# Kernel optimization log

Measured on AMD Instinct MI355X. Metric: run time of the kernel, lower is better.

Reference implementation:

```python
import jax, jax.numpy as jnp
import numpy as np

MAX_SX = 10  # max_shiftx
MAX_SY = 10  # max_shifty
STD_EPS = 1e-9


def setup_inputs() -> dict:
    key = jax.random.key(0)
    x = jax.random.normal(key, (8, 32, 128, 128), dtype=jnp.float32)
    return {"x": x}


def _cross_correlation(x):
    b, c, h, w = x.shape
    n = h * w
    # _standartize: zero-mean, divide by (unbiased std * sqrt(h*w)); std<eps -> inf -> 0
    xc = x - jnp.mean(x, axis=(2, 3), keepdims=True)
    std = jnp.std(xc, axis=(2, 3), keepdims=True, ddof=1)
    std = jnp.where(std < STD_EPS, jnp.inf, std)
    xs = xc / (std * jnp.sqrt(jnp.asarray(n, x.dtype)))
    # FFT-based circular cross-correlation for all ordered pairs (i, j>=i)
    Xf = jnp.fft.fft2(xs)  # [b, c, h, w] complex
    ii, jj = np.triu_indices(c)  # row-major: (0,0),(0,1),...,(0,c-1),(1,1),... matches the loop order
    cross = Xf[:, ii] * jnp.conj(Xf[:, jj])  # [b, P, h, w], P = c*(c+1)//2
    cc = jnp.real(jnp.fft.ifft2(cross))
    # The [[br, bl], [tr, tl]] corner concat == roll by (sy, sx) then take leading window
    cc = jnp.roll(cc, (MAX_SY, MAX_SX), axis=(2, 3))
    return cc[:, :, : 2 * MAX_SY + 1, : 2 * MAX_SX + 1]  # [b, P, 2sy+1, 2sx+1]


def reference(x):
    return _cross_correlation(x)
```

## Files before the change

kernel.cpp:

```cpp
#include <hip/hip_runtime.h>
#include <hip/hip_bf16.h>

typedef __attribute__((ext_vector_type(4))) unsigned int uint4v;
typedef __attribute__((ext_vector_type(8))) short short8;
typedef __attribute__((ext_vector_type(16))) float floatx16;

#define NROWP 152
#define ROWB2 12288
#define BB2   ((size_t)NROWP*ROWB2)
#define COPYB ((size_t)8*BB2)
#define STATS_OFF ((size_t)2*COPYB)
#define ABUF (38*2048)
#define LDS_BYTES (2*ABUF)

__device__ __forceinline__ unsigned short f2b(float f){
  unsigned int u = __float_as_uint(f);
  return (unsigned short)((u + 0x7fffu + ((u >> 16) & 1u)) >> 16);
}

__device__ __forceinline__ void gload_lds16(const void* g, void* l){
  __builtin_amdgcn_global_load_lds((const __attribute__((address_space(1))) unsigned int*)g,
                                   (__attribute__((address_space(3))) unsigned int*)l, 16, 0, 0);
}

__global__ __launch_bounds__(256) void k_stat(const float* __restrict__ x,
                                              float* __restrict__ stats){
  int bid = blockIdx.x;
  int t = threadIdx.x;
  const float* xc = x + ((size_t)bid << 14);
  float s = 0.f, ss = 0.f;
  #pragma unroll 4
  for (int k = 0; k < 64; ++k){
    float v = xc[t + (k << 8)];
    s += v; ss += v*v;
  }
  #pragma unroll
  for (int m = 32; m >= 1; m >>= 1){
    s  += __shfl_xor(s, m);
    ss += __shfl_xor(ss, m);
  }
  __shared__ float rs[4], rss[4];
  int wv = t >> 6, l = t & 63;
  if (l == 0){ rs[wv] = s; rss[wv] = ss; }
  __syncthreads();
  if (t == 0){
    float S  = rs[0]+rs[1]+rs[2]+rs[3];
    float SS = rss[0]+rss[1]+rss[2]+rss[3];
    float mean = S * (1.f/16384.f);
    float var  = (SS - S*mean) * (1.f/16383.f);
    float sd = sqrtf(fmaxf(var, 0.f));
    stats[bid*2]   = mean;
    stats[bid*2+1] = (sd < 1e-9f) ? 0.f : 1.f/(sd*128.f);
  }
}

__global__ __launch_bounds__(512) void k_pack(const float* __restrict__ x,
                                              const float* __restrict__ stats,
                                              unsigned char* __restrict__ pad){
  __shared__ float rowbuf[32*129];
  int bid = blockIdx.x;
  int b = bid & 7, rg = bid >> 3;
  int t = threadIdx.x;
  int ch = t >> 4, xq = t & 15;
  float mean  = stats[(b*32 + ch)*2];
  float scale = stats[(b*32 + ch)*2 + 1];
  const float* xc = x + ((size_t)(b*32 + ch) << 14);
  for (int rr = 0; rr < 4; ++rr){
    int r = rg*4 + rr;
    int sy = (r + 118) & 127;
    const float* src = xc + (sy << 7) + (xq << 3);
    float4 v0 = *(const float4*)src;
    float4 v1 = *(const float4*)(src + 4);
    float* rb = rowbuf + ch*129 + (xq << 3);
    rb[0] = (v0.x-mean)*scale; rb[1] = (v0.y-mean)*scale;
    rb[2] = (v0.z-mean)*scale; rb[3] = (v0.w-mean)*scale;
    rb[4] = (v1.x-mean)*scale; rb[5] = (v1.y-mean)*scale;
    rb[6] = (v1.z-mean)*scale; rb[7] = (v1.w-mean)*scale;
    __syncthreads();
    #pragma unroll
    for (int k = 0; k < 3; ++k){
      int u = t + (k << 9);
      int pp = (u >= 768) ? 1 : 0;
      int u2 = u - 768*pp;
      int xi = u2 / 192;
      int u3 = u2 - 192*xi;
      int cq = u3 / 6;
      int seg = u3 - 6*cq;
      const float* rbq = rowbuf + cq*129;
      int x0 = 32*xi + 8*seg + pp;
      unsigned int d[4];
      #pragma unroll
      for (int e = 0; e < 4; ++e){
        unsigned int lo = f2b(rbq[(x0 + 2*e)     & 127]);
        unsigned int hi = f2b(rbq[(x0 + 2*e + 1) & 127]);
        d[e] = lo | (hi << 16);
      }
      uint4v ov = {d[0], d[1], d[2], d[3]};
      *(uint4v*)(pad + (size_t)pp*COPYB + ((size_t)(b*NROWP + r))*ROWB2
                 + (unsigned)(xi*3072 + cq*96 + seg*16)) = ov;
    }
    __syncthreads();
  }
}

__global__ __launch_bounds__(512, 1) void k_corr(const unsigned char* __restrict__ pad,
                                                 float* __restrict__ out){
  extern __shared__ char lds[];
  float* sf = (float*)lds;

  int bid = blockIdx.x;
  int b = bid & 7, cg = bid >> 3;
  int dx, d0;
  if (cg < 2){ dx = 0; d0 = cg << 2; }
  else { int q = cg - 2; dx = 1 + q/3; d0 = -10 + 7*(q - 3*(q/3)); }
  int p = dx & 1, dxe = dx - p;

  int tid = threadIdx.x;
  int lane = tid & 63, wvi = tid >> 6;
  int ks = wvi & 1, kq = wvi >> 1;
  unsigned offF = (unsigned)(ks*1024 + ((lane >> 5) << 9) + ((lane & 31) << 4));
  unsigned oA = (unsigned)((lane & 31)*96 + 2*dxe);
  unsigned oB = (unsigned)((lane & 31)*96 + 16*(2*ks + (lane >> 5)));

  const unsigned char* baseA = pad + (size_t)p*COPYB + (size_t)b*BB2;
  const unsigned char* baseB = pad + (size_t)b*BB2;

  floatx16 acc[7];
  #pragma unroll
  for (int d = 0; d < 7; ++d) acc[d] = (floatx16)(0.0f);

  auto stageA = [&](int tt, char* buf){
    int rab = 32*(tt >> 2) + 10 + d0;
    unsigned xio = (unsigned)((tt & 3)*3072);
    #pragma unroll
    for (int s = 0; s < 10; ++s){
      int u = wvi + (s << 3);
      if (s < 9 || wvi < 4){
        int row = u >> 1, cp = u & 1;
        const unsigned char* g = baseA + (size_t)(rab + row)*ROWB2 + xio
                                 + oA + (unsigned)(16*(2*cp + (lane >> 5)));
        gload_lds16(g, buf + (unsigned)(row*2048 + cp*1024 + lane*16));
      }
    }
  };
  auto pBrow = [&](int tt)->const unsigned char*{
    return baseB + (size_t)(32*(tt >> 2) + 10 + kq*8)*ROWB2
                 + (unsigned)((tt & 3)*3072) + oB;
  };

  stageA(0, lds);
  __builtin_amdgcn_sched_barrier(0);
  short8 BQ[4];
  {
    const unsigned char* pB0 = pBrow(0);
    #pragma unroll
    for (int k = 0; k < 4; ++k) __builtin_memcpy(&BQ[k], pB0 + (size_t)k*ROWB2, 16);
  }
  __builtin_amdgcn_sched_barrier(0);
  asm volatile("s_waitcnt vmcnt(4)" ::: "memory");
  __builtin_amdgcn_sched_barrier(0);
  __builtin_amdgcn_s_barrier();
  __builtin_amdgcn_sched_barrier(0);

  for (int t = 0; t < 16; ++t){
    if (t < 15) stageA(t+1, lds + ((t+1)&1)*ABUF);
    __builtin_amdgcn_sched_barrier(0);
    const char* Ab = lds + (t&1)*ABUF + (kq*8)*2048 + offF;
    const unsigned char* pBc = pBrow(t);
    const unsigned char* pBn = pBrow(t+1);
    bool more = (t < 15);
    short8 ring[8];
    #pragma unroll
    for (int w = 0; w < 8; ++w) ring[w] = *(const short8*)(Ab + w*2048);
    __builtin_amdgcn_s_setprio(1);
    #pragma unroll
    for (int yl = 0; yl < 8; ++yl){
      short8 bf = BQ[yl & 3];
      #pragma unroll
      for (int d = 0; d < 7; ++d)
        acc[d] = __builtin_amdgcn_mfma_f32_32x32x16_bf16(ring[(yl+d)&7], bf, acc[d], 0, 0, 0);
      if (yl < 4)       __builtin_memcpy(&BQ[yl & 3], pBc + (size_t)(yl + 4)*ROWB2, 16);
      else if (more)    __builtin_memcpy(&BQ[yl & 3], pBn + (size_t)(yl - 4)*ROWB2, 16);
      if (yl < 6) ring[yl & 7] = *(const short8*)(Ab + (yl + 8)*2048);
    }
    __builtin_amdgcn_s_setprio(0);
    __builtin_amdgcn_sched_barrier(0);
    asm volatile("s_waitcnt vmcnt(4) lgkmcnt(0)" ::: "memory");
    __builtin_amdgcn_sched_barrier(0);
    __builtin_amdgcn_s_barrier();
    __builtin_amdgcn_sched_barrier(0);
  }

  int baseb = b * 232848;
  #pragma unroll
  for (int d = 0; d < 7; ++d){
    #pragma unroll
    for (int r = 0; r < 16; ++r)
      sf[wvi*1024 + r*64 + lane] = acc[d][r];
    __syncthreads();
    int dy = d0 + d;
    #pragma unroll
    for (int k = 0; k < 2; ++k){
      int pp0 = tid + (k << 9);
      float v = 0.f;
      #pragma unroll
      for (int w = 0; w < 8; ++w) v += sf[w*1024 + pp0];
      int reg = pp0 >> 6, ln = pp0 & 63;
      int i = (reg & 3) + 8*(reg >> 2) + 4*(ln >> 5);
      int j = ln & 31;
      if (i <= j){
        int pp = i*(65 - i)/2 + (j - i);
        out[baseb + pp*441 + (10+dy)*21 + (10+dx)] = v;
        if (i == j && (dy != 0 || dx != 0))
          out[baseb + pp*441 + (10-dy)*21 + (10-dx)] = v;
      } else {
        int pp = j*(65 - j)/2 + (i - j);
        out[baseb + pp*441 + (10-dy)*21 + (10-dx)] = v;
      }
    }
    __syncthreads();
  }
}

extern "C" void kernel_launch(void* const* d_in, const int* in_sizes, int n_in,
                              void* d_out, int out_size, void* d_ws, size_t ws_size,
                              hipStream_t stream){
  const float* x = (const float*)d_in[0];
  unsigned char* pad = (unsigned char*)d_ws;
  float* stats = (float*)((char*)d_ws + STATS_OFF);
  float* out = (float*)d_out;
  hipFuncSetAttribute((const void*)k_corr, hipFuncAttributeMaxDynamicSharedMemorySize,
                      LDS_BYTES);
  k_stat<<<dim3(256), dim3(256), 0, stream>>>(x, stats);
  k_pack<<<dim3(304), dim3(512), 0, stream>>>(x, stats, pad);
  k_corr<<<dim3(256), dim3(512), LDS_BYTES, stream>>>(pad, out);
}
```

Before: 82.56 us.

## Interleave A-tile staging with MFMA phases using barrier-synchronized ping-pong schedule

Splits each iteration's A-tile global-to-LDS staging into four chunks, each issued between pairs of MFMA steps, with workgroup barriers separating the memory and compute phases. This is a ping-pong style schedule meant to overlap global loads with matrix math and spread memory traffic evenly. It adds several barriers per iteration, which can cost synchronization time. It also changes the vmcnt wait accounting, which could hurt correctness or throughput if the counts are off.

Result: no change. 83.16 us (+0.7%).

```diff
diff --git a/kernel.cpp b/kernel.cpp
--- a/kernel.cpp
+++ b/kernel.cpp
@@ -12,6 +12,8 @@
 #define STATS_OFF ((size_t)2*COPYB)
 #define ABUF (38*2048)
 #define LDS_BYTES (2*ABUF)
+
+#define SB __builtin_amdgcn_sched_barrier(0)
 
 __device__ __forceinline__ unsigned short f2b(float f){
   unsigned int u = __float_as_uint(f);
@@ -129,18 +131,14 @@
   #pragma unroll
   for (int d = 0; d < 7; ++d) acc[d] = (floatx16)(0.0f);
 
-  auto stageA = [&](int tt, char* buf){
-    int rab = 32*(tt >> 2) + 10 + d0;
-    unsigned xio = (unsigned)((tt & 3)*3072);
-    #pragma unroll
-    for (int s = 0; s < 10; ++s){
-      int u = wvi + (s << 3);
-      if (s < 9 || wvi < 4){
-        int row = u >> 1, cp = u & 1;
-        const unsigned char* g = baseA + (size_t)(rab + row)*ROWB2 + xio
-                                 + oA + (unsigned)(16*(2*cp + (lane >> 5)));
-        gload_lds16(g, buf + (unsigned)(row*2048 + cp*1024 + lane*16));
-      }
+  auto stageUnit = [&](int tt, char* buf, int s){
+    int u = wvi + (s << 3);
+    if (u < 76){
+      int row = u >> 1, cp = u & 1;
+      int rab = 32*(tt >> 2) + 10 + d0;
+      const unsigned char* g = baseA + (size_t)(rab + row)*ROWB2
+            + (unsigned)((tt & 3)*3072) + oA + (unsigned)(16*(2*cp + (lane >> 5)));
+      gload_lds16(g, buf + (unsigned)(row*2048 + cp*1024 + lane*16));
     }
   };
   auto pBrow = [&](int tt)->const unsigned char*{
@@ -148,47 +146,74 @@
                  + (unsigned)((tt & 3)*3072) + oB;
   };
 
-  stageA(0, lds);
-  __builtin_amdgcn_sched_barrier(0);
+  #pragma unroll
+  for (int s = 0; s < 10; ++s) stageUnit(0, lds, s);
+  SB;
   short8 BQ[4];
   {
     const unsigned char* pB0 = pBrow(0);
     #pragma unroll
     for (int k = 0; k < 4; ++k) __builtin_memcpy(&BQ[k], pB0 + (size_t)k*ROWB2, 16);
   }
-  __builtin_amdgcn_sched_barrier(0);
+  SB;
   asm volatile("s_waitcnt vmcnt(4)" ::: "memory");
-  __builtin_amdgcn_sched_barrier(0);
-  __builtin_amdgcn_s_barrier();
-  __builtin_amdgcn_sched_barrier(0);
+  SB; __builtin_amdgcn_s_barrier(); SB;
 
   for (int t = 0; t < 16; ++t){
-    if (t < 15) stageA(t+1, lds + ((t+1)&1)*ABUF);
-    __builtin_amdgcn_sched_barrier(0);
     const char* Ab = lds + (t&1)*ABUF + (kq*8)*2048 + offF;
+    char* nbuf = lds + ((t+1)&1)*ABUF;
     const unsigned char* pBc = pBrow(t);
     const unsigned char* pBn = pBrow(t+1);
     bool more = (t < 15);
     short8 ring[8];
-    #pragma unroll
-    for (int w = 0; w < 8; ++w) ring[w] = *(const short8*)(Ab + w*2048);
-    __builtin_amdgcn_s_setprio(1);
-    #pragma unroll
-    for (int yl = 0; yl < 8; ++yl){
+    auto STEP = [&](int yl){
       short8 bf = BQ[yl & 3];
       #pragma unroll
       for (int d = 0; d < 7; ++d)
         acc[d] = __builtin_amdgcn_mfma_f32_32x32x16_bf16(ring[(yl+d)&7], bf, acc[d], 0, 0, 0);
-      if (yl < 4)       __builtin_memcpy(&BQ[yl & 3], pBc + (size_t)(yl + 4)*ROWB2, 16);
-      else if (more)    __builtin_memcpy(&BQ[yl & 3], pBn + (size_t)(yl - 4)*ROWB2, 16);
-      if (yl < 6) ring[yl & 7] = *(const short8*)(Ab + (yl + 8)*2048);
-    }
-    __builtin_amdgcn_s_setprio(0);
-    __builtin_amdgcn_sched_barrier(0);
-    asm volatile("s_waitcnt vmcnt(4) lgkmcnt(0)" ::: "memory");
-    __builtin_amdgcn_sched_barrier(0);
-    __builtin_amdgcn_s_barrier();
-    __builtin_amdgcn_sched_barrier(0);
+    };
+    #pragma unroll
+    for (int w = 0; w < 8; ++w) ring[w] = *(const short8*)(Ab + w*2048);
+    if (more){ stageUnit(t+1,nbuf,0); stageUnit(t+1,nbuf,1); stageUnit(t+1,nbuf,2); }
+    SB; __builtin_amdgcn_s_barrier();
+    asm volatile("s_waitcnt lgkmcnt(0)" ::: "memory"); SB;
+    __builtin_amdgcn_s_setprio(1); STEP(0); STEP(1); __builtin_amdgcn_s_setprio(0);
+    __builtin_memcpy(&BQ[0], pBc + (size_t)4*ROWB2, 16);
+    __builtin_memcpy(&BQ[1], pBc + (size_t)5*ROWB2, 16);
+    SB; __builtin_amdgcn_s_barrier(); SB;
+    ring[0] = *(const short8*)(Ab + 8*2048);
+    ring[1] = *(const short8*)(Ab + 9*2048);
+    if (more){ stageUnit(t+1,nbuf,3); stageUnit(t+1,nbuf,4); stageUnit(t+1,nbuf,5); }
+    SB; __builtin_amdgcn_s_barrier();
+    asm volatile("s_waitcnt lgkmcnt(0)" ::: "memory"); SB;
+    __builtin_amdgcn_s_setprio(1); STEP(2); STEP(3); __builtin_amdgcn_s_setprio(0);
+    __builtin_memcpy(&BQ[2], pBc + (size_t)6*ROWB2, 16);
+    __builtin_memcpy(&BQ[3], pBc + (size_t)7*ROWB2, 16);
+    SB; __builtin_amdgcn_s_barrier(); SB;
+    ring[2] = *(const short8*)(Ab + 10*2048);
+    ring[3] = *(const short8*)(Ab + 11*2048);
+    if (more){ stageUnit(t+1,nbuf,6); stageUnit(t+1,nbuf,7); }
+    SB; __builtin_amdgcn_s_barrier();
+    asm volatile("s_waitcnt lgkmcnt(0)" ::: "memory"); SB;
+    __builtin_amdgcn_s_setprio(1); STEP(4); STEP(5); __builtin_amdgcn_s_setprio(0);
+    if (more){
+      __builtin_memcpy(&BQ[0], pBn, 16);
+      __builtin_memcpy(&BQ[1], pBn + (size_t)ROWB2, 16);
+    }
+    SB; __builtin_amdgcn_s_barrier(); SB;
+    ring[4] = *(const short8*)(Ab + 12*2048);
+    ring[5] = *(const short8*)(Ab + 13*2048);
+    if (more){ stageUnit(t+1,nbuf,8); stageUnit(t+1,nbuf,9); }
+    SB; __builtin_amdgcn_s_barrier();
+    asm volatile("s_waitcnt lgkmcnt(0)" ::: "memory"); SB;
+    __builtin_amdgcn_s_setprio(1); STEP(6); STEP(7); __builtin_amdgcn_s_setprio(0);
+    if (more){
+      __builtin_memcpy(&BQ[2], pBn + (size_t)2*ROWB2, 16);
+      __builtin_memcpy(&BQ[3], pBn + (size_t)3*ROWB2, 16);
+    }
+    SB;
+    if (more){ asm volatile("s_waitcnt vmcnt(2)" ::: "memory"); }
+    SB; __builtin_amdgcn_s_barrier(); SB;
   }
 
   int baseb = b * 232848;
```

## Fuse channel statistics into pack and apply normalization algebraically in epilogue

Applied to the files above, without the earlier changes.

Removes the separate statistics kernel that re-read the whole input: the pack kernel now stores raw bf16 values and accumulates per-channel partial sums and sums of squares. A tiny single-block kernel reduces those partials to mean and scale. The correlation epilogue then corrects each output as (sum - N*mean_i*mean_j)*scale_i*scale_j. This saves a full pass over the input, at the cost of an extra small serial launch and some precision risk, since raw values rather than centered ones are rounded to bf16.

Result: faster. 79.19 us (-4.1%).

```diff
diff --git a/kernel.cpp b/kernel.cpp
--- a/kernel.cpp
+++ b/kernel.cpp
@@ -9,9 +9,12 @@
 #define ROWB2 12288
 #define BB2   ((size_t)NROWP*ROWB2)
 #define COPYB ((size_t)8*BB2)
-#define STATS_OFF ((size_t)2*COPYB)
+#define PART_OFF ((size_t)2*COPYB)
+#define STATS_OFF (PART_OFF + 304*32*2*4)
 #define ABUF (38*2048)
 #define LDS_BYTES (2*ABUF)
+
+#define SB __builtin_amdgcn_sched_barrier(0)
 
 __device__ __forceinline__ unsigned short f2b(float f){
   unsigned int u = __float_as_uint(f);
@@ -23,59 +26,30 @@
                                    (__attribute__((address_space(3))) unsigned int*)l, 16, 0, 0);
 }
 
-__global__ __launch_bounds__(256) void k_stat(const float* __restrict__ x,
-                                              float* __restrict__ stats){
-  int bid = blockIdx.x;
-  int t = threadIdx.x;
-  const float* xc = x + ((size_t)bid << 14);
-  float s = 0.f, ss = 0.f;
-  #pragma unroll 4
-  for (int k = 0; k < 64; ++k){
-    float v = xc[t + (k << 8)];
-    s += v; ss += v*v;
-  }
-  #pragma unroll
-  for (int m = 32; m >= 1; m >>= 1){
-    s  += __shfl_xor(s, m);
-    ss += __shfl_xor(ss, m);
-  }
-  __shared__ float rs[4], rss[4];
-  int wv = t >> 6, l = t & 63;
-  if (l == 0){ rs[wv] = s; rss[wv] = ss; }
-  __syncthreads();
-  if (t == 0){
-    float S  = rs[0]+rs[1]+rs[2]+rs[3];
-    float SS = rss[0]+rss[1]+rss[2]+rss[3];
-    float mean = S * (1.f/16384.f);
-    float var  = (SS - S*mean) * (1.f/16383.f);
-    float sd = sqrtf(fmaxf(var, 0.f));
-    stats[bid*2]   = mean;
-    stats[bid*2+1] = (sd < 1e-9f) ? 0.f : 1.f/(sd*128.f);
-  }
-}
-
 __global__ __launch_bounds__(512) void k_pack(const float* __restrict__ x,
-                                              const float* __restrict__ stats,
-                                              unsigned char* __restrict__ pad){
+                                              unsigned char* __restrict__ pad,
+                                              float* __restrict__ part){
   __shared__ float rowbuf[32*129];
   int bid = blockIdx.x;
   int b = bid & 7, rg = bid >> 3;
   int t = threadIdx.x;
   int ch = t >> 4, xq = t & 15;
-  float mean  = stats[(b*32 + ch)*2];
-  float scale = stats[(b*32 + ch)*2 + 1];
   const float* xc = x + ((size_t)(b*32 + ch) << 14);
+  float s = 0.f, ss = 0.f;
   for (int rr = 0; rr < 4; ++rr){
     int r = rg*4 + rr;
     int sy = (r + 118) & 127;
     const float* src = xc + (sy << 7) + (xq << 3);
     float4 v0 = *(const float4*)src;
     float4 v1 = *(const float4*)(src + 4);
+    if (r >= 10 && r < 138){
+      s  += v0.x+v0.y+v0.z+v0.w + v1.x+v1.y+v1.z+v1.w;
+      ss += v0.x*v0.x+v0.y*v0.y+v0.z*v0.z+v0.w*v0.w
+          + v1.x*v1.x+v1.y*v1.y+v1.z*v1.z+v1.w*v1.w;
+    }
     float* rb = rowbuf + ch*129 + (xq << 3);
-    rb[0] = (v0.x-mean)*scale; rb[1] = (v0.y-mean)*scale;
-    rb[2] = (v0.z-mean)*scale; rb[3] = (v0.w-mean)*scale;
-    rb[4] = (v1.x-mean)*scale; rb[5] = (v1.y-mean)*scale;
-    rb[6] = (v1.z-mean)*scale; rb[7] = (v1.w-mean)*scale;
+    rb[0] = v0.x; rb[1] = v0.y; rb[2] = v0.z; rb[3] = v0.w;
+    rb[4] = v1.x; rb[5] = v1.y; rb[6] = v1.z; rb[7] = v1.w;
     __syncthreads();
     #pragma unroll
     for (int k = 0; k < 3; ++k){
@@ -101,9 +75,37 @@
     }
     __syncthreads();
   }
+  #pragma unroll
+  for (int m = 8; m >= 1; m >>= 1){
+    s  += __shfl_xor(s, m);
+    ss += __shfl_xor(ss, m);
+  }
+  if (xq == 0){
+    part[(bid*32 + ch)*2]     = s;
+    part[(bid*32 + ch)*2 + 1] = ss;
+  }
+}
+
+__global__ __launch_bounds__(256) void k_stat2(const float* __restrict__ part,
+                                               float* __restrict__ stats){
+  int t = threadIdx.x;
+  int b = t >> 5, c = t & 31;
+  float S = 0.f, SS = 0.f;
+  #pragma unroll
+  for (int rg = 0; rg < 38; ++rg){
+    int idx = (((rg << 3) + b)*32 + c)*2;
+    S  += part[idx];
+    SS += part[idx + 1];
+  }
+  float mean = S * (1.f/16384.f);
+  float var  = (SS - S*mean) * (1.f/16383.f);
+  float sd = sqrtf(fmaxf(var, 0.f));
+  stats[t*2]   = mean;
+  stats[t*2+1] = (sd < 1e-9f) ? 0.f : 1.f/(sd*128.f);
 }
 
 __global__ __launch_bounds__(512, 1) void k_corr(const unsigned char* __restrict__ pad,
+                                                 const float* __restrict__ stats,
                                                  float* __restrict__ out){
   extern __shared__ char lds[];
   float* sf = (float*)lds;
@@ -149,22 +151,20 @@
   };
 
   stageA(0, lds);
-  __builtin_amdgcn_sched_barrier(0);
+  SB;
   short8 BQ[4];
   {
     const unsigned char* pB0 = pBrow(0);
     #pragma unroll
     for (int k = 0; k < 4; ++k) __builtin_memcpy(&BQ[k], pB0 + (size_t)k*ROWB2, 16);
   }
-  __builtin_amdgcn_sched_barrier(0);
+  SB;
   asm volatile("s_waitcnt vmcnt(4)" ::: "memory");
-  __builtin_amdgcn_sched_barrier(0);
-  __builtin_amdgcn_s_barrier();
-  __builtin_amdgcn_sched_barrier(0);
+  SB; __builtin_amdgcn_s_barrier(); SB;
 
   for (int t = 0; t < 16; ++t){
     if (t < 15) stageA(t+1, lds + ((t+1)&1)*ABUF);
-    __builtin_amdgcn_sched_barrier(0);
+    SB;
     const char* Ab = lds + (t&1)*ABUF + (kq*8)*2048 + offF;
     const unsigned char* pBc = pBrow(t);
     const unsigned char* pBn = pBrow(t+1);
@@ -184,14 +184,13 @@
       if (yl < 6) ring[yl & 7] = *(const short8*)(Ab + (yl + 8)*2048);
     }
     __builtin_amdgcn_s_setprio(0);
-    __builtin_amdgcn_sched_barrier(0);
+    SB;
     asm volatile("s_waitcnt vmcnt(4) lgkmcnt(0)" ::: "memory");
-    __builtin_amdgcn_sched_barrier(0);
-    __builtin_amdgcn_s_barrier();
-    __builtin_amdgcn_sched_barrier(0);
+    SB; __builtin_amdgcn_s_barrier(); SB;
   }
 
   int baseb = b * 232848;
+  const float* st = stats + b*64;
   #pragma unroll
   for (int d = 0; d < 7; ++d){
     #pragma unroll
@@ -202,12 +201,15 @@
     #pragma unroll
     for (int k = 0; k < 2; ++k){
       int pp0 = tid + (k << 9);
-      float v = 0.f;
+      float v0 = 0.f;
       #pragma unroll
-      for (int w = 0; w < 8; ++w) v += sf[w*1024 + pp0];
+      for (int w = 0; w < 8; ++w) v0 += sf[w*1024 + pp0];
       int reg = pp0 >> 6, ln = pp0 & 63;
       int i = (reg & 3) + 8*(reg >> 2) + 4*(ln >> 5);
       int j = ln & 31;
+      float mi = st[2*i], si = st[2*i+1];
+      float mj = st[2*j], sj = st[2*j+1];
+      float v = (v0 - 16384.f*mi*mj) * (si*sj);
       if (i <= j){
         int pp = i*(65 - i)/2 + (j - i);
         out[baseb + pp*441 + (10+dy)*21 + (10+dx)] = v;
@@ -227,11 +229,12 @@
                               hipStream_t stream){
   const float* x = (const float*)d_in[0];
   unsigned char* pad = (unsigned char*)d_ws;
+  float* part  = (float*)((char*)d_ws + PART_OFF);
   float* stats = (float*)((char*)d_ws + STATS_OFF);
   float* out = (float*)d_out;
   hipFuncSetAttribute((const void*)k_corr, hipFuncAttributeMaxDynamicSharedMemorySize,
                       LDS_BYTES);
-  k_stat<<<dim3(256), dim3(256), 0, stream>>>(x, stats);
-  k_pack<<<dim3(304), dim3(512), 0, stream>>>(x, stats, pad);
-  k_corr<<<dim3(256), dim3(512), LDS_BYTES, stream>>>(pad, out);
-}
+  k_pack<<<dim3(304), dim3(512), 0, stream>>>(x, pad, part);
+  k_stat2<<<dim3(1), dim3(256), 0, stream>>>(part, stats);
+  k_corr<<<dim3(256), dim3(512), LDS_BYTES, stream>>>(pad, stats, out);
+}
```
